# Kernel tuning notes

Measured on AMD Instinct MI355X. Metric: run time of the kernel, lower is better.

Reference implementation:

```python
import jax, jax.numpy as jnp
import numpy as np
import math

FACTOR = 5

def setup_inputs() -> dict:
    key = jax.random.key(0)
    k1, k2, k3, k4 = jax.random.split(key, 4)
    B, L, H, D = 8, 4096, 8, 64
    sample_k = FACTOR * int(np.ceil(np.log(L)))  # 45
    return {
        "queries": jax.random.normal(k1, (B, L, H, D), dtype=jnp.float32),
        "keys": jax.random.normal(k2, (B, L, H, D), dtype=jnp.float32),
        "values": jax.random.normal(k3, (B, L, H, D), dtype=jnp.float32),
        "index_sample": jax.random.randint(k4, (L, sample_k), 0, L, dtype=jnp.int64),
    }


def reference(queries, keys, values, index_sample):
    B, L_Q, H, D = queries.shape
    L_K = keys.shape[1]
    # [B, H, L, D]
    Q = jnp.transpose(queries, (0, 2, 1, 3))
    K = jnp.transpose(keys, (0, 2, 1, 3))
    V = jnpp = jnp.transpose(values, (0, 2, 1, 3))

    u = min(FACTOR * int(math.ceil(math.log(L_Q))), L_Q)  # n_top

    # --- _prob_QK ---
    # sampled keys: [B, H, L_Q, sample_k, D]
    K_sample = K[:, :, index_sample, :]
    # Q_K_sample: [B, H, L_Q, sample_k]
    Q_K_sample = jnp.einsum("bhqd,bhqsd->bhqs", Q, K_sample)
    M = jnp.max(Q_K_sample, axis=-1) - jnp.sum(Q_K_sample, axis=-1) / L_K
    _, M_top = jax.lax.top_k(M, u)  # [B, H, u]
    Q_reduce = jnp.take_along_axis(Q, M_top[..., None], axis=2)  # [B, H, u, D]
    scores = jnp.einsum("bhud,bhkd->bhuk", Q_reduce, K)  # [B, H, u, L_K]

    scale = 1.0 / math.sqrt(D)
    scores = scores * scale

    # --- initial context (mask_flag=True): causal cumsum of V ---
    context = jnp.cumsum(V, axis=2)  # [B, H, L_V, D]

    # --- causal ProbMask: key position j invalid if j > query position ---
    key_pos = jnp.arange(L_K)
    mask = key_pos[None, None, None, :] > M_top[..., None]  # [B, H, u, L_K]
    scores = jnp.where(mask, -jnp.inf, scores)

    attn = jax.nn.softmax(scores, axis=-1)  # dropout is identity at eval
    values_agg = jnp.einsum("bhuk,bhkd->bhud", attn, V)  # [B, H, u, D]

    b_idx = jnp.arange(B)[:, None, None]
    h_idx = jnp.arange(H)[None, :, None]
    context = context.at[b_idx, h_idx, M_top].set(values_agg)

    return jnp.transpose(context, (0, 2, 1, 3))  # [B, L_Q, H, D]
```

## Files before the change

kernel.cpp:

```cpp
#include <hip/hip_runtime.h>
#include <math.h>

#define Bc 8
#define Lc 4096
#define Hc 8
#define Dc 64
#define NCH 8
#define VCH 16
#define VROWS (Lc / VCH)

__constant__ int c_cb[NCH + 1] = {0, 256, 576, 832, 1216, 1600, 2048, 2624, 4096};

template<int CTRL>
__device__ __forceinline__ float dpp_mov(float v) {
    return __int_as_float(__builtin_amdgcn_update_dpp(
        0, __float_as_int(v), CTRL, 0xF, 0xF, true));
}
template<int CTRL>
__device__ __forceinline__ float dpp_radd(float v) {
    return v + dpp_mov<CTRL>(v);
}
__device__ __forceinline__ float row16_sum(float p) {
    p = dpp_radd<0x128>(p); p = dpp_radd<0x124>(p);
    p = dpp_radd<0x122>(p); p = dpp_radd<0x121>(p);
    return p;
}
__device__ __forceinline__ float wmax64(float v) {
    v = fmaxf(v, dpp_mov<0x128>(v));
    v = fmaxf(v, dpp_mov<0x124>(v));
    v = fmaxf(v, dpp_mov<0x122>(v));
    v = fmaxf(v, dpp_mov<0x121>(v));
    v = fmaxf(v, __shfl_xor(v, 16, 64));
    return fmaxf(v, __shfl_xor(v, 32, 64));
}
__device__ __forceinline__ float wsum64(float v) {
    v = row16_sum(v);
    v += __shfl_xor(v, 16, 64);
    return v + __shfl_xor(v, 32, 64);
}

template<int S>
__global__ __launch_bounds__(256) void k_meas_t(
    const float* __restrict__ Q, const float* __restrict__ K,
    const int* __restrict__ idx, float* __restrict__ M)
{
    constexpr int NIT = (S + 3) / 4;
    int b = blockIdx.z, h = blockIdx.y;
    int w = threadIdx.x >> 6, lane = threadIdx.x & 63;
    int q = blockIdx.x * 4 + w;
    int grp = lane >> 4, gl = lane & 15;

    const float4 qv = *(const float4*)(Q + (((size_t)b * Lc + q) * Hc + h) * Dc + gl * 4);
    const int* ip = idx + (size_t)q * S + grp;
    const float* Kb = K + ((size_t)b * Lc * Hc + h) * Dc + gl * 4;

    int rows[NIT];
    #pragma unroll
    for (int it = 0; it < NIT - 1; it++) rows[it] = ip[it * 4];
    {
        int s = 4 * (NIT - 1) + grp;
        rows[NIT - 1] = ip[(s < S) ? 4 * (NIT - 1) : (S - 1 - grp)];
    }

    float mloc = -INFINITY, sloc = 0.f;
    #pragma unroll
    for (int it = 0; it < NIT; it++) {
        const float4 kw = *(const float4*)(Kb + ((size_t)rows[it] << 9));
        float p = kw.x * qv.x + kw.y * qv.y + kw.z * qv.z + kw.w * qv.w;
        p = row16_sum(p);
        int s = it * 4 + grp;
        if (s < S) { mloc = fmaxf(mloc, p); sloc += p; }
    }
    mloc = fmaxf(mloc, __shfl_xor(mloc, 16, 64));
    mloc = fmaxf(mloc, __shfl_xor(mloc, 32, 64));
    sloc += __shfl_xor(sloc, 16, 64);
    sloc += __shfl_xor(sloc, 32, 64);

    if (lane == 0)
        M[((size_t)(b * Hc + h)) * Lc + q] = mloc - sloc * (1.0f / (float)Lc);
}

__global__ __launch_bounds__(256) void k_meas_dyn(
    const float* __restrict__ Q, const float* __restrict__ K,
    const int* __restrict__ idx, float* __restrict__ M, int S)
{
    int b = blockIdx.z, h = blockIdx.y;
    int w = threadIdx.x >> 6, lane = threadIdx.x & 63;
    int q = blockIdx.x * 4 + w;
    int grp = lane >> 4, gl = lane & 15;

    const float4 qv = *(const float4*)(Q + (((size_t)b * Lc + q) * Hc + h) * Dc + gl * 4);
    const int* ip = idx + (size_t)q * S;
    const float* Kb = K + ((size_t)b * Lc * Hc + h) * Dc + gl * 4;

    float mloc = -INFINITY, sloc = 0.f;
    int niter = (S + 3) >> 2;
    for (int it = 0; it < niter; it++) {
        int s = it * 4 + grp;
        int ii = s < S ? s : S - 1;
        int row = ip[ii];
        const float4 kw = *(const float4*)(Kb + ((size_t)row << 9));
        float p = kw.x * qv.x + kw.y * qv.y + kw.z * qv.z + kw.w * qv.w;
        p = row16_sum(p);
        if (s < S) { mloc = fmaxf(mloc, p); sloc += p; }
    }
    mloc = fmaxf(mloc, __shfl_xor(mloc, 16, 64));
    mloc = fmaxf(mloc, __shfl_xor(mloc, 32, 64));
    sloc += __shfl_xor(sloc, 16, 64);
    sloc += __shfl_xor(sloc, 32, 64);
    if (lane == 0)
        M[((size_t)(b * Hc + h)) * Lc + q] = mloc - sloc * (1.0f / (float)Lc);
}

__global__ __launch_bounds__(256) void k_topk(
    const float* __restrict__ M, int* __restrict__ top, int U)
{
    int bh = blockIdx.x;
    int tid = threadIdx.x;
    const float* m = M + (size_t)bh * Lc;

    unsigned long long key[16];
    #pragma unroll
    for (int j = 0; j < 16; j++) {
        int i = tid * 16 + j;
        unsigned int u = __float_as_uint(m[i]);
        u ^= (unsigned int)(((int)u >> 31)) | 0x80000000u;
        key[j] = ((unsigned long long)u << 32) | (unsigned int)i;
    }
    unsigned long long myb = key[0];
    #pragma unroll
    for (int j = 1; j < 16; j++) myb = key[j] > myb ? key[j] : myb;

    __shared__ unsigned long long swave[2][4];

    for (int u = 0; u < U; u++) {
        unsigned long long wmax = myb;
        #pragma unroll
        for (int o = 32; o >= 1; o >>= 1) {
            unsigned long long t = __shfl_xor(wmax, o, 64);
            wmax = t > wmax ? t : wmax;
        }
        if ((tid & 63) == 0) swave[u & 1][tid >> 6] = wmax;
        __syncthreads();
        unsigned long long w0 = swave[u & 1][0], w1 = swave[u & 1][1];
        unsigned long long w2 = swave[u & 1][2], w3 = swave[u & 1][3];
        unsigned long long a = w0 > w1 ? w0 : w1;
        unsigned long long c = w2 > w3 ? w2 : w3;
        unsigned long long win = a > c ? a : c;
        int widx = (int)(win & 0xFFFFFFFFu);
        if (tid == 0) top[(size_t)bh * U + u] = widx;
        if (tid == (widx >> 4)) {
            #pragma unroll
            for (int j = 0; j < 16; j++) if (j == (widx & 15)) key[j] = 0ull;
            unsigned long long b2 = key[0];
            #pragma unroll
            for (int j = 1; j < 16; j++) b2 = key[j] > b2 ? key[j] : b2;
            myb = b2;
        }
    }
}

__global__ __launch_bounds__(256) void k_vsum(
    const float* __restrict__ V, float* __restrict__ bsum)
{
    int b = blockIdx.z, h = blockIdx.y, c = blockIdx.x;
    int d = threadIdx.x & 63, g = threadIdx.x >> 6;
    __shared__ float part[4][64];
    float s = 0.f;
    int r0 = c * VROWS;
    for (int r = r0 + g; r < r0 + VROWS; r += 4)
        s += V[(((size_t)b * Lc + r) * Hc + h) * Dc + d];
    part[g][d] = s;
    __syncthreads();
    if (g == 0)
        bsum[(((size_t)(b * Hc + h)) * VCH + c) * 64 + d] =
            part[0][d] + part[1][d] + part[2][d] + part[3][d];
}

__global__ __launch_bounds__(256) void k_scan(
    const float* __restrict__ V, const float* __restrict__ bsum,
    float* __restrict__ out)
{
    int b = blockIdx.z, h = blockIdx.y, c = blockIdx.x;
    int d = threadIdx.x & 63, g = threadIdx.x >> 6;
    int bh = b * Hc + h;
    __shared__ float gtot[4][64];
    __shared__ float goff[4][64];

    float base = 0.f;
    for (int cc = 0; cc < c; cc++)
        base += bsum[((size_t)bh * VCH + cc) * 64 + d];

    int gs = c * VROWS + g * 64;
    float gsum = 0.f;
    for (int r = gs; r < gs + 64; r++)
        gsum += V[(((size_t)b * Lc + r) * Hc + h) * Dc + d];
    gtot[g][d] = gsum;
    __syncthreads();
    if (g == 0) {
        float run = base;
        for (int gg = 0; gg < 4; gg++) { goff[gg][d] = run; run += gtot[gg][d]; }
    }
    __syncthreads();
    float run = goff[g][d];
    for (int r = gs; r < gs + 64; r++) {
        size_t o = (((size_t)b * Lc + r) * Hc + h) * Dc + d;
        run += V[o];
        out[o] = run;
    }
}

__global__ __launch_bounds__(256) void k_attn2(
    const float* __restrict__ Q, const float* __restrict__ K,
    const float* __restrict__ V, const int* __restrict__ top,
    float* __restrict__ Opart, float* __restrict__ Mp, float* __restrict__ Lp,
    int U)
{
    int b = blockIdx.z, h = blockIdx.y, c = blockIdx.x;
    int bh = b * Hc + h;
    int tid = threadIdx.x;
    int lane = tid & 63, g = tid >> 6;

    __shared__ float4 sK4[64][16];
    __shared__ float  sVT[64][65];
    __shared__ float  sQ[45][64];
    __shared__ float  sP[45][64];
    __shared__ int    sqi[45];

    if (tid < U) sqi[tid] = top[(size_t)bh * U + tid];
    __syncthreads();
    for (int u = g; u < U; u += 4)
        sQ[u][lane] = Q[(((size_t)b * Lc + sqi[u]) * Hc + h) * Dc + lane] * 0.125f;

    int qbm = 0;
    for (int u = 0; u < U; u++) qbm = max(qbm, sqi[u]);

    int qq[16], tt[16];
    int ulast = g + (((U - 1 - g) >> 2) << 2);
    #pragma unroll
    for (int i = 0; i < 12; i++) {
        int u = g + 4 * i;
        u = (u <= ulast) ? u : ulast;
        tt[i] = u; qq[i] = sqi[u];
    }
    #pragma unroll
    for (int i = 12; i < 16; i++) { tt[i] = tt[11]; qq[i] = 0x7FFFFFFF; }
    #pragma unroll
    for (int kk = 2; kk <= 16; kk <<= 1) {
        #pragma unroll
        for (int jj = kk >> 1; jj > 0; jj >>= 1) {
            #pragma unroll
            for (int ii = 0; ii < 16; ii++) {
                int ll = ii ^ jj;
                if (ll > ii) {
                    bool up = ((ii & kk) == 0);
                    bool sw = up ? (qq[ii] > qq[ll]) : (qq[ii] < qq[ll]);
                    if (sw) {
                        int tq = qq[ii]; qq[ii] = qq[ll]; qq[ll] = tq;
                        int tu = tt[ii]; tt[ii] = tt[ll]; tt[ll] = tu;
                    }
                }
            }
        }
    }

    float m_r[12], l_r[12], o_r[12];
    #pragma unroll
    for (int j = 0; j < 12; j++) { m_r[j] = -INFINITY; l_r[j] = 0.f; o_r[j] = 0.f; }

    int k0c = c_cb[c], k1c = c_cb[c + 1];
    int ntile = 0;
    if (qbm >= k0c) {
        int lastk = min(qbm, k1c - 1);
        ntile = (lastk - k0c) / 64 + 1;
    }
    int kswz = lane & 7;

    for (int t = 0; t < ntile; t++) {
        int k0 = k0c + t * 64;
        __syncthreads();
        {
            const float* kp = K + (((size_t)b * Lc + k0 + lane) * Hc + h) * Dc + g * 16;
            const float* vp = V + (((size_t)b * Lc + k0 + lane) * Hc + h) * Dc + g * 16;
            #pragma unroll
            for (int i = 0; i < 4; i++) {
                float4 kw = *(const float4*)(kp + i * 4);
                float4 vw = *(const float4*)(vp + i * 4);
                int lb = g * 4 + i;
                sK4[lane][lb ^ (lane & 7)] = kw;
                int d0 = lb * 4;
                sVT[d0+0][lane] = vw.x; sVT[d0+1][lane] = vw.y;
                sVT[d0+2][lane] = vw.z; sVT[d0+3][lane] = vw.w;
            }
        }
        __syncthreads();

        #pragma unroll
        for (int j0 = 0; j0 < 12; j0 += 4) {
            if (k0 > qq[j0 + 3]) continue;
            int ua = tt[j0], ub = tt[j0+1], uc = tt[j0+2], ud = tt[j0+3];
            float s0 = 0.f, s1 = 0.f, s2 = 0.f, s3 = 0.f;
            #pragma unroll
            for (int lb = 0; lb < 16; lb++) {
                float4 kb = sK4[lane][lb ^ kswz];
                float4 qa = *(const float4*)&sQ[ua][lb * 4];
                float4 qb = *(const float4*)&sQ[ub][lb * 4];
                float4 qc = *(const float4*)&sQ[uc][lb * 4];
                float4 qd = *(const float4*)&sQ[ud][lb * 4];
                s0 += kb.x*qa.x + kb.y*qa.y + kb.z*qa.z + kb.w*qa.w;
                s1 += kb.x*qb.x + kb.y*qb.y + kb.z*qb.z + kb.w*qb.w;
                s2 += kb.x*qc.x + kb.y*qc.y + kb.z*qc.z + kb.w*qc.w;
                s3 += kb.x*qd.x + kb.y*qd.y + kb.z*qd.z + kb.w*qd.w;
            }
            float a0, a1, a2, a3;
#define SLOT(jj, sv, av) { \
            float sA = (k0 + lane > qq[jj]) ? -INFINITY : sv; \
            float tm = wmax64(sA); \
            float mnew = fmaxf(m_r[jj], tm); \
            float p = __expf(sA - mnew); \
            float ps = wsum64(p); \
            av = __expf(m_r[jj] - mnew); \
            m_r[jj] = mnew; \
            l_r[jj] = l_r[jj] * av + ps; \
            sP[tt[jj]][lane] = p; }
            SLOT(j0+0, s0, a0)
            SLOT(j0+1, s1, a1)
            SLOT(j0+2, s2, a2)
            SLOT(j0+3, s3, a3)
#undef SLOT
            float p0 = 0.f, p1 = 0.f, p2 = 0.f, p3 = 0.f;
            #pragma unroll
            for (int k = 0; k < 64; k += 4) {
                float v0 = sVT[lane][k+0], v1 = sVT[lane][k+1];
                float v2 = sVT[lane][k+2], v3 = sVT[lane][k+3];
                float4 wa = *(const float4*)&sP[ua][k];
                float4 wb = *(const float4*)&sP[ub][k];
                float4 wc = *(const float4*)&sP[uc][k];
                float4 wd = *(const float4*)&sP[ud][k];
                p0 += wa.x*v0 + wa.y*v1 + wa.z*v2 + wa.w*v3;
                p1 += wb.x*v0 + wb.y*v1 + wb.z*v2 + wb.w*v3;
                p2 += wc.x*v0 + wc.y*v1 + wc.z*v2 + wc.w*v3;
                p3 += wd.x*v0 + wd.y*v1 + wd.z*v2 + wd.w*v3;
            }
            o_r[j0+0] = o_r[j0+0] * a0 + p0;
            o_r[j0+1] = o_r[j0+1] * a1 + p1;
            o_r[j0+2] = o_r[j0+2] * a2 + p2;
            o_r[j0+3] = o_r[j0+3] * a3 + p3;
        }
    }

    #pragma unroll
    for (int j = 0; j < 12; j++) {
        int u = tt[j];
        size_t s0 = ((size_t)bh * NCH + c) * U + u;
        Opart[s0 * 64 + lane] = o_r[j];
        if (lane == 0) { Mp[s0] = m_r[j]; Lp[s0] = l_r[j]; }
    }
}

__global__ __launch_bounds__(64) void k_combine(
    const float* __restrict__ Opart, const float* __restrict__ Mp,
    const float* __restrict__ Lp, const int* __restrict__ top,
    float* __restrict__ out, int U)
{
    int b = blockIdx.z, h = blockIdx.y, u = blockIdx.x;
    int bh = b * Hc + h;
    int lane = threadIdx.x;
    int q = top[(size_t)bh * U + u];

    float mv[NCH], lv[NCH];
    float mg = -INFINITY;
    #pragma unroll
    for (int c = 0; c < NCH; c++) {
        size_t s0 = ((size_t)bh * NCH + c) * U + u;
        mv[c] = Mp[s0]; lv[c] = Lp[s0];
        mg = fmaxf(mg, mv[c]);
    }
    float Ls = 0.f, o = 0.f;
    #pragma unroll
    for (int c = 0; c < NCH; c++) {
        if (lv[c] > 0.f) {
            float w = __expf(mv[c] - mg);
            Ls += w * lv[c];
            o  += w * Opart[(((size_t)bh * NCH + c) * U + u) * 64 + lane];
        }
    }
    out[(((size_t)b * Lc + q) * Hc + h) * Dc + lane] = o / Ls;
}

extern "C" void kernel_launch(void* const* d_in, const int* in_sizes, int n_in,
                              void* d_out, int out_size, void* d_ws, size_t ws_size,
                              hipStream_t stream)
{
    const float* Q = (const float*)d_in[0];
    const float* K = (const float*)d_in[1];
    const float* V = (const float*)d_in[2];
    const int* idx = (const int*)d_in[3];
    float* out = (float*)d_out;

    int S = in_sizes[3] / Lc;

    char* ws = (char*)d_ws;
    float* M     = (float*)ws;
    float* Opart = (float*)ws;
    float* Mp    = (float*)(ws + 6291456);
    float* Lp    = (float*)(ws + 6422528);
    float* bsum  = (float*)(ws + 6815744);
    int*   top   = (int*)  (ws + 8388608);

    dim3 blk(256);
    if (S == 45)
        k_meas_t<45><<<dim3(Lc / 4, Hc, Bc), blk, 0, stream>>>(Q, K, idx, M);
    else
        k_meas_dyn  <<<dim3(Lc / 4, Hc, Bc), blk, 0, stream>>>(Q, K, idx, M, S);
    k_topk   <<<dim3(Bc * Hc),        blk, 0, stream>>>(M, top, S);
    k_vsum   <<<dim3(VCH, Hc, Bc),    blk, 0, stream>>>(V, bsum);
    k_scan   <<<dim3(VCH, Hc, Bc),    blk, 0, stream>>>(V, bsum, out);
    k_attn2  <<<dim3(NCH, Hc, Bc),    blk, 0, stream>>>(Q, K, V, top, Opart, Mp, Lp, S);
    k_combine<<<dim3(S, Hc, Bc), dim3(64), 0, stream>>>(Opart, Mp, Lp, top, out, S);
}
```

Before: 636.2 us.

## Sort top-k indices in topk kernel and split attention blocks by query slices

The top-k kernel now collects the selected indices in shared memory and sorts them ascending with an odd-even transposition sort before writing them out. The attention kernel is split across query slices of 16, which gives more blocks. Each wave handles 4 consecutive sorted queries, so the per-block bitonic sort and the 12-slot register arrays go away and causal tile skipping becomes tighter. The V tile is stored with a swizzled float4 layout in place of a padded transpose. The cost is that K/V tiles are reloaded once per query slice, and the serial sort adds U barriers to the top-k kernel.

```diff
diff --git a/kernel.cpp b/kernel.cpp
--- a/kernel.cpp
+++ b/kernel.cpp
@@ -6,6 +6,7 @@
 #define Hc 8
 #define Dc 64
 #define NCH 8
+#define QB 16
 #define VCH 16
 #define VROWS (Lc / VCH)
 
@@ -132,6 +133,7 @@
     for (int j = 1; j < 16; j++) myb = key[j] > myb ? key[j] : myb;
 
     __shared__ unsigned long long swave[2][4];
+    __shared__ int swin[256];
 
     for (int u = 0; u < U; u++) {
         unsigned long long wmax = myb;
@@ -148,7 +150,7 @@
         unsigned long long c = w2 > w3 ? w2 : w3;
         unsigned long long win = a > c ? a : c;
         int widx = (int)(win & 0xFFFFFFFFu);
-        if (tid == 0) top[(size_t)bh * U + u] = widx;
+        if (tid == 0) swin[u] = widx;
         if (tid == (widx >> 4)) {
             #pragma unroll
             for (int j = 0; j < 16; j++) if (j == (widx & 15)) key[j] = 0ull;
@@ -158,6 +160,16 @@
             myb = b2;
         }
     }
+    __syncthreads();
+    for (int ph = 0; ph < U; ph++) {
+        int i = 2 * tid + (ph & 1);
+        if (i + 1 < U) {
+            int a = swin[i], b2 = swin[i + 1];
+            if (a > b2) { swin[i] = b2; swin[i + 1] = a; }
+        }
+        __syncthreads();
+    }
+    if (tid < U) top[(size_t)bh * U + tid] = swin[tid];
 }
 
 __global__ __launch_bounds__(256) void k_vsum(
@@ -216,57 +228,35 @@
     float* __restrict__ Opart, float* __restrict__ Mp, float* __restrict__ Lp,
     int U)
 {
-    int b = blockIdx.z, h = blockIdx.y, c = blockIdx.x;
+    int b = blockIdx.z, h = blockIdx.y;
+    int c = blockIdx.x % NCH, s = blockIdx.x / NCH;
     int bh = b * Hc + h;
     int tid = threadIdx.x;
     int lane = tid & 63, g = tid >> 6;
 
     __shared__ float4 sK4[64][16];
-    __shared__ float  sVT[64][65];
-    __shared__ float  sQ[45][64];
-    __shared__ float  sP[45][64];
-    __shared__ int    sqi[45];
-
-    if (tid < U) sqi[tid] = top[(size_t)bh * U + tid];
+    __shared__ float4 sV4[64][16];
+    __shared__ float  sQ[QB][64];
+    __shared__ float  sP[QB][64];
+
+    int* sqi = (int*)&sP[0][0];
+
+    int u0 = s * QB;
+    int nu = min(QB, U - u0);
+    if (tid < nu) sqi[tid] = top[(size_t)bh * U + u0 + tid];
     __syncthreads();
-    for (int u = g; u < U; u += 4)
+    for (int u = g; u < nu; u += 4)
         sQ[u][lane] = Q[(((size_t)b * Lc + sqi[u]) * Hc + h) * Dc + lane] * 0.125f;
 
-    int qbm = 0;
-    for (int u = 0; u < U; u++) qbm = max(qbm, sqi[u]);
-
-    int qq[16], tt[16];
-    int ulast = g + (((U - 1 - g) >> 2) << 2);
-    #pragma unroll
-    for (int i = 0; i < 12; i++) {
-        int u = g + 4 * i;
-        u = (u <= ulast) ? u : ulast;
-        tt[i] = u; qq[i] = sqi[u];
-    }
-    #pragma unroll
-    for (int i = 12; i < 16; i++) { tt[i] = tt[11]; qq[i] = 0x7FFFFFFF; }
-    #pragma unroll
-    for (int kk = 2; kk <= 16; kk <<= 1) {
-        #pragma unroll
-        for (int jj = kk >> 1; jj > 0; jj >>= 1) {
-            #pragma unroll
-            for (int ii = 0; ii < 16; ii++) {
-                int ll = ii ^ jj;
-                if (ll > ii) {
-                    bool up = ((ii & kk) == 0);
-                    bool sw = up ? (qq[ii] > qq[ll]) : (qq[ii] < qq[ll]);
-                    if (sw) {
-                        int tq = qq[ii]; qq[ii] = qq[ll]; qq[ll] = tq;
-                        int tu = tt[ii]; tt[ii] = tt[ll]; tt[ll] = tu;
-                    }
-                }
-            }
-        }
-    }
-
-    float m_r[12], l_r[12], o_r[12];
-    #pragma unroll
-    for (int j = 0; j < 12; j++) { m_r[j] = -INFINITY; l_r[j] = 0.f; o_r[j] = 0.f; }
+    int qbm = sqi[nu - 1];
+    int nu1 = nu - 1;
+    int l0 = min(4 * g + 0, nu1), l1 = min(4 * g + 1, nu1);
+    int l2 = min(4 * g + 2, nu1), l3 = min(4 * g + 3, nu1);
+    int q0 = sqi[l0], q1 = sqi[l1], q2 = sqi[l2], q3 = sqi[l3];
+
+    float m0 = -INFINITY, m1 = -INFINITY, m2 = -INFINITY, m3 = -INFINITY;
+    float L0 = 0.f, L1 = 0.f, L2 = 0.f, L3 = 0.f;
+    float o0 = 0.f, o1 = 0.f, o2 = 0.f, o3 = 0.f;
 
     int k0c = c_cb[c], k1c = c_cb[c + 1];
     int ntile = 0;
@@ -287,75 +277,75 @@
                 float4 kw = *(const float4*)(kp + i * 4);
                 float4 vw = *(const float4*)(vp + i * 4);
                 int lb = g * 4 + i;
-                sK4[lane][lb ^ (lane & 7)] = kw;
+                sK4[lane][lb ^ kswz] = kw;
                 int d0 = lb * 4;
-                sVT[d0+0][lane] = vw.x; sVT[d0+1][lane] = vw.y;
-                sVT[d0+2][lane] = vw.z; sVT[d0+3][lane] = vw.w;
+                ((float*)&sV4[d0 + 0][(lane >> 2) ^ ((d0 + 0) & 7)])[lane & 3] = vw.x;
+                ((float*)&sV4[d0 + 1][(lane >> 2) ^ ((d0 + 1) & 7)])[lane & 3] = vw.y;
+                ((float*)&sV4[d0 + 2][(lane >> 2) ^ ((d0 + 2) & 7)])[lane & 3] = vw.z;
+                ((float*)&sV4[d0 + 3][(lane >> 2) ^ ((d0 + 3) & 7)])[lane & 3] = vw.w;
             }
         }
         __syncthreads();
 
-        #pragma unroll
-        for (int j0 = 0; j0 < 12; j0 += 4) {
-            if (k0 > qq[j0 + 3]) continue;
-            int ua = tt[j0], ub = tt[j0+1], uc = tt[j0+2], ud = tt[j0+3];
+        if (k0 <= q3) {
             float s0 = 0.f, s1 = 0.f, s2 = 0.f, s3 = 0.f;
             #pragma unroll
             for (int lb = 0; lb < 16; lb++) {
                 float4 kb = sK4[lane][lb ^ kswz];
-                float4 qa = *(const float4*)&sQ[ua][lb * 4];
-                float4 qb = *(const float4*)&sQ[ub][lb * 4];
-                float4 qc = *(const float4*)&sQ[uc][lb * 4];
-                float4 qd = *(const float4*)&sQ[ud][lb * 4];
+                float4 qa = *(const float4*)&sQ[l0][lb * 4];
+                float4 qb = *(const float4*)&sQ[l1][lb * 4];
+                float4 qc = *(const float4*)&sQ[l2][lb * 4];
+                float4 qd = *(const float4*)&sQ[l3][lb * 4];
                 s0 += kb.x*qa.x + kb.y*qa.y + kb.z*qa.z + kb.w*qa.w;
                 s1 += kb.x*qb.x + kb.y*qb.y + kb.z*qb.z + kb.w*qb.w;
                 s2 += kb.x*qc.x + kb.y*qc.y + kb.z*qc.z + kb.w*qc.w;
                 s3 += kb.x*qd.x + kb.y*qd.y + kb.z*qd.z + kb.w*qd.w;
             }
             float a0, a1, a2, a3;
-#define SLOT(jj, sv, av) { \
-            float sA = (k0 + lane > qq[jj]) ? -INFINITY : sv; \
+#define SLOT(li, qi, sv, mv, lv, av) { \
+            float sA = (k0 + lane > qi) ? -INFINITY : sv; \
             float tm = wmax64(sA); \
-            float mnew = fmaxf(m_r[jj], tm); \
+            float mnew = fmaxf(mv, tm); \
             float p = __expf(sA - mnew); \
             float ps = wsum64(p); \
-            av = __expf(m_r[jj] - mnew); \
-            m_r[jj] = mnew; \
-            l_r[jj] = l_r[jj] * av + ps; \
-            sP[tt[jj]][lane] = p; }
-            SLOT(j0+0, s0, a0)
-            SLOT(j0+1, s1, a1)
-            SLOT(j0+2, s2, a2)
-            SLOT(j0+3, s3, a3)
+            av = __expf(mv - mnew); \
+            mv = mnew; \
+            lv = lv * av + ps; \
+            sP[li][lane] = p; }
+            SLOT(l0, q0, s0, m0, L0, a0)
+            SLOT(l1, q1, s1, m1, L1, a1)
+            SLOT(l2, q2, s2, m2, L2, a2)
+            SLOT(l3, q3, s3, m3, L3, a3)
 #undef SLOT
             float p0 = 0.f, p1 = 0.f, p2 = 0.f, p3 = 0.f;
             #pragma unroll
-            for (int k = 0; k < 64; k += 4) {
-                float v0 = sVT[lane][k+0], v1 = sVT[lane][k+1];
-                float v2 = sVT[lane][k+2], v3 = sVT[lane][k+3];
-                float4 wa = *(const float4*)&sP[ua][k];
-                float4 wb = *(const float4*)&sP[ub][k];
-                float4 wc = *(const float4*)&sP[uc][k];
-                float4 wd = *(const float4*)&sP[ud][k];
-                p0 += wa.x*v0 + wa.y*v1 + wa.z*v2 + wa.w*v3;
-                p1 += wb.x*v0 + wb.y*v1 + wb.z*v2 + wb.w*v3;
-                p2 += wc.x*v0 + wc.y*v1 + wc.z*v2 + wc.w*v3;
-                p3 += wd.x*v0 + wd.y*v1 + wd.z*v2 + wd.w*v3;
+            for (int kk = 0; kk < 16; kk++) {
+                float4 vb = sV4[lane][kk ^ kswz];
+                float4 wa = *(const float4*)&sP[l0][kk * 4];
+                float4 wb = *(const float4*)&sP[l1][kk * 4];
+                float4 wc = *(const float4*)&sP[l2][kk * 4];
+                float4 wd = *(const float4*)&sP[l3][kk * 4];
+                p0 += wa.x*vb.x + wa.y*vb.y + wa.z*vb.z + wa.w*vb.w;
+                p1 += wb.x*vb.x + wb.y*vb.y + wb.z*vb.z + wb.w*vb.w;
+                p2 += wc.x*vb.x + wc.y*vb.y + wc.z*vb.z + wc.w*vb.w;
+                p3 += wd.x*vb.x + wd.y*vb.y + wd.z*vb.z + wd.w*vb.w;
             }
-            o_r[j0+0] = o_r[j0+0] * a0 + p0;
-            o_r[j0+1] = o_r[j0+1] * a1 + p1;
-            o_r[j0+2] = o_r[j0+2] * a2 + p2;
-            o_r[j0+3] = o_r[j0+3] * a3 + p3;
-        }
-    }
-
-    #pragma unroll
-    for (int j = 0; j < 12; j++) {
-        int u = tt[j];
-        size_t s0 = ((size_t)bh * NCH + c) * U + u;
-        Opart[s0 * 64 + lane] = o_r[j];
-        if (lane == 0) { Mp[s0] = m_r[j]; Lp[s0] = l_r[j]; }
-    }
+            o0 = o0 * a0 + p0;
+            o1 = o1 * a1 + p1;
+            o2 = o2 * a2 + p2;
+            o3 = o3 * a3 + p3;
+        }
+    }
+
+#define WR(li, mv, lv, ov) { \
+    size_t s0_ = ((size_t)bh * NCH + c) * U + (u0 + li); \
+    Opart[s0_ * 64 + lane] = ov; \
+    if (lane == 0) { Mp[s0_] = mv; Lp[s0_] = lv; } }
+    WR(l0, m0, L0, o0)
+    WR(l1, m1, L1, o1)
+    WR(l2, m2, L2, o2)
+    WR(l3, m3, L3, o3)
+#undef WR
 }
 
 __global__ __launch_bounds__(64) void k_combine(
@@ -399,6 +389,7 @@
     float* out = (float*)d_out;
 
     int S = in_sizes[3] / Lc;
+    int QSL = (S + QB - 1) / QB;
 
     char* ws = (char*)d_ws;
     float* M     = (float*)ws;
@@ -413,9 +404,9 @@
         k_meas_t<45><<<dim3(Lc / 4, Hc, Bc), blk, 0, stream>>>(Q, K, idx, M);
     else
         k_meas_dyn  <<<dim3(Lc / 4, Hc, Bc), blk, 0, stream>>>(Q, K, idx, M, S);
-    k_topk   <<<dim3(Bc * Hc),        blk, 0, stream>>>(M, top, S);
-    k_vsum   <<<dim3(VCH, Hc, Bc),    blk, 0, stream>>>(V, bsum);
-    k_scan   <<<dim3(VCH, Hc, Bc),    blk, 0, stream>>>(V, bsum, out);
-    k_attn2  <<<dim3(NCH, Hc, Bc),    blk, 0, stream>>>(Q, K, V, top, Opart, Mp, Lp, S);
+    k_topk   <<<dim3(Bc * Hc),          blk, 0, stream>>>(M, top, S);
+    k_vsum   <<<dim3(VCH, Hc, Bc),      blk, 0, stream>>>(V, bsum);
+    k_scan   <<<dim3(VCH, Hc, Bc),      blk, 0, stream>>>(V, bsum, out);
+    k_attn2  <<<dim3(NCH * QSL, Hc, Bc), blk, 0, stream>>>(Q, K, V, top, Opart, Mp, Lp, S);
     k_combine<<<dim3(S, Hc, Bc), dim3(64), 0, stream>>>(Opart, Mp, Lp, top, out, S);
 }
```

New measurement: 668.2 us. 1.05x slower.
